# Performance work log

Measured on AMD Instinct MI355X. Metric: run time of the kernel, lower is better.

Reference implementation:

```python
import jax, jax.numpy as jnp
import numpy as np

LL = 1 << 20            # Fastfood padded size (power of 2 >= DD)
DD = 1024 * 768         # out_features * in_features
OUT, IN = 1024, 768


def fwht(v):
    """Unnormalized fast Walsh-Hadamard transform over a length-2^k vector."""
    n = v.shape[0]
    h = 1
    while h < n:
        v = v.reshape(-1, 2, h)
        v = jnp.concatenate([v[:, 0] + v[:, 1], v[:, 0] - v[:, 1]], axis=-1)
        h *= 2
    return v.reshape(n)


def setup_inputs() -> dict:
    key = jax.random.key(0)
    ks = jax.random.split(key, 7)
    x = jax.random.normal(ks[0], (8, 2048, IN), dtype=jnp.float32)
    theta = jax.random.normal(ks[1], (2048,), dtype=jnp.float32)
    W_0 = jax.random.normal(ks[2], (OUT, IN), dtype=jnp.float32) * 0.02
    b = jax.random.normal(ks[3], (OUT,), dtype=jnp.float32) * 0.02
    # Rademacher +/-1 diagonal
    BB = (jax.random.bernoulli(ks[4], 0.5, (LL,)).astype(jnp.float32) * 2.0 - 1.0)
    GG = jax.random.normal(ks[5], (LL,), dtype=jnp.float32)
    Pi = jax.random.permutation(ks[6], LL).astype(jnp.int64)
    return {"x": x, "theta": theta, "W_0": W_0, "b": b, "BB": BB, "GG": GG, "Pi": Pi}


def reference(x, theta, W_0, b, BB, GG, Pi):
    # pad intrinsic parameter to LL (theta.numel() < LL branch)
    theta_pad = jnp.zeros((LL,), dtype=theta.dtype).at[: theta.shape[0]].set(theta)
    # Fastfood: H B theta -> permute -> G diag -> H
    v = fwht(BB * theta_pad)
    v = v[Pi] * GG
    v = fwht(v)
    divisor = jnp.sqrt(LL * jnp.sum(GG * GG))
    update_vec = v[:DD] / (divisor * np.sqrt(float(DD) / LL))
    W_eff = W_0 + update_vec.reshape(OUT, IN)
    return jnp.einsum("bsi,oi->bso", x, W_eff) + b
```

## Files before the change

kernel.cpp:

```cpp
#include <hip/hip_runtime.h>
#include <hip/hip_bf16.h>


#define LL (1 << 20)
#define DD (1024 * 768)
#define OUTF 1024
#define INF 768
#define MROWS 16384

typedef __attribute__((ext_vector_type(8))) short s16x8;
typedef __attribute__((ext_vector_type(4))) float f32x4;
typedef __attribute__((ext_vector_type(16))) float f32x16;

__device__ __forceinline__ unsigned short f2bf(float f) {
    union { float f; unsigned u; } v; v.f = f;
    unsigned r = v.u + 0x7FFF + ((v.u >> 16) & 1);
    return (unsigned short)(r >> 16);
}

__global__ void k3_gather_fwht_lo(const int* __restrict__ Pi, const float* __restrict__ GG,
                                  const float* __restrict__ BB, const float* __restrict__ theta,
                                  const float* __restrict__ X, ushort* __restrict__ XB,
                                  float* __restrict__ T, float* __restrict__ partial) {
    __shared__ float s[1024];
    __shared__ float r01s[2048];
    __shared__ float ws4[4];
    const int tid = threadIdx.x;
    const int row = blockIdx.x;
    const int4   pv = ((const int4*)Pi)[row * 256 + tid];
    const float4 gv = ((const float4*)GG)[row * 256 + tid];
    for (int j = tid; j < 2048; j += 256) r01s[j] = BB[j] * theta[j];
    for (int h = 1; h < 1024; h <<= 1) {
        __syncthreads();
        for (int w = tid; w < 1024; w += 256) {
            int rr = w >> 9;
            int b  = w & 511;
            int bh = b & (h - 1);
            int i  = ((b - bh) << 1) + bh + rr * 1024;
            float a = r01s[i], c = r01s[i + h];
            r01s[i] = a + c; r01s[i + h] = a - c;
        }
    }
    float g2 = gv.x * gv.x + gv.y * gv.y + gv.z * gv.z + gv.w * gv.w;
    #pragma unroll
    for (int o = 32; o > 0; o >>= 1) g2 += __shfl_down(g2, o, 64);
    if ((tid & 63) == 0) ws4[tid >> 6] = g2;
    __syncthreads();
    {
        int p; float g, v;
        p = pv.x; g = gv.x;
        v = (r01s[p & 1023] + (((p >> 10) & 1) ? -1.0f : 1.0f) * r01s[1024 + (p & 1023)]) * g;
        s[tid * 4 + 0] = v;
        p = pv.y; g = gv.y;
        v = (r01s[p & 1023] + (((p >> 10) & 1) ? -1.0f : 1.0f) * r01s[1024 + (p & 1023)]) * g;
        s[tid * 4 + 1] = v;
        p = pv.z; g = gv.z;
        v = (r01s[p & 1023] + (((p >> 10) & 1) ? -1.0f : 1.0f) * r01s[1024 + (p & 1023)]) * g;
        s[tid * 4 + 2] = v;
        p = pv.w; g = gv.w;
        v = (r01s[p & 1023] + (((p >> 10) & 1) ? -1.0f : 1.0f) * r01s[1024 + (p & 1023)]) * g;
        s[tid * 4 + 3] = v;
    }
    for (int h = 1; h < 1024; h <<= 1) {
        __syncthreads();
        for (int w = tid; w < 512; w += 256) {
            int bh = w & (h - 1);
            int i  = ((w - bh) << 1) + bh;
            float a = s[i], c = s[i + h];
            s[i] = a + c; s[i + h] = a - c;
        }
    }
    __syncthreads();
    float4 v;
    v.x = s[tid * 4 + 0]; v.y = s[tid * 4 + 1]; v.z = s[tid * 4 + 2]; v.w = s[tid * 4 + 3];
    ((float4*)T)[row * 256 + tid] = v;
    if (tid == 0) partial[row] = ws4[0] + ws4[1] + ws4[2] + ws4[3];

    const float4* X4 = (const float4*)X + (size_t)row * 3072;
    ushort4* XB4 = (ushort4*)XB + (size_t)row * 3072;
    #pragma unroll
    for (int j = 0; j < 12; j++) {
        float4 xv = X4[j * 256 + tid];
        ushort4 o;
        o.x = f2bf(xv.x); o.y = f2bf(xv.y); o.z = f2bf(xv.z); o.w = f2bf(xv.w);
        XB4[j * 256 + tid] = o;
    }
}

__global__ void k4_fwht_hi(const float* __restrict__ T, const float* __restrict__ partial,
                           const float* __restrict__ W0, ushort* __restrict__ WB) {
    __shared__ float s[8 * 1025];
    __shared__ float rw[5];
    const int tid = threadIdx.x;
    float p = partial[tid] + partial[tid + 256] + partial[tid + 512] + partial[tid + 768];
    #pragma unroll
    for (int o = 32; o > 0; o >>= 1) p += __shfl_down(p, o, 64);
    if ((tid & 63) == 0) rw[tid >> 6] = p;

    const int lo0 = blockIdx.x * 8;
    const float4* T4 = (const float4*)T;
    const int hio = tid >> 1;
    const int q   = tid & 1;
    for (int hb = 0; hb < 8; hb++) {
        int hi = hb * 128 + hio;
        float4 v = T4[hi * 256 + (lo0 >> 2) + q];
        s[(4 * q + 0) * 1025 + hi] = v.x;
        s[(4 * q + 1) * 1025 + hi] = v.y;
        s[(4 * q + 2) * 1025 + hi] = v.z;
        s[(4 * q + 3) * 1025 + hi] = v.w;
    }
    __syncthreads();
    if (tid == 0) rw[4] = rw[0] + rw[1] + rw[2] + rw[3];
    for (int h = 1; h < 1024; h <<= 1) {
        for (int w = tid; w < 8 * 512; w += 256) {
            int col = w >> 9;
            int b   = w & 511;
            int bh  = b & (h - 1);
            int i   = ((b - bh) << 1) + bh;
            float* pp = s + col * 1025;
            float a = pp[i], c = pp[i + h];
            pp[i] = a + c; pp[i + h] = a - c;
        }
        __syncthreads();
    }
    const float scale = rsqrtf(rw[4] * (float)DD);
    for (int hb = 0; hb < 6; hb++) {
        int hi = hb * 128 + hio;
        int d  = hi * 1024 + lo0 + 4 * q;
        float4 w = *(const float4*)&W0[d];
        ushort4 o;
        o.x = f2bf(w.x + s[(4 * q + 0) * 1025 + hi] * scale);
        o.y = f2bf(w.y + s[(4 * q + 1) * 1025 + hi] * scale);
        o.z = f2bf(w.z + s[(4 * q + 2) * 1025 + hi] * scale);
        o.w = f2bf(w.w + s[(4 * q + 3) * 1025 + hi] * scale);
        *(ushort4*)&WB[d] = o;
    }
}

#define BM 128
#define BN 128
#define BK 64

__global__ __launch_bounds__(256)
void k7_gemm(const ushort* __restrict__ A, const ushort* __restrict__ B,
             const float* __restrict__ bias, float* __restrict__ C) {
    __shared__ ushort As[BM * BK];
    __shared__ ushort Bs[BN * BK];
    const int tid  = threadIdx.x;
    const int lane = tid & 63;
    const int wave = tid >> 6;
    const int m0 = blockIdx.x * BM;
    const int n0 = blockIdx.y * BN;
    const int wm = (wave & 1) * 64;
    const int wn = (wave >> 1) * 64;

    const int fr_row = lane & 31;
    const int fr_kh  = lane >> 5;

    f32x16 acc[2][2];
    #pragma unroll
    for (int i = 0; i < 2; i++)
        #pragma unroll
        for (int j = 0; j < 2; j++) acc[i][j] = (f32x16)(0.0f);

    for (int kt = 0; kt < INF; kt += BK) {
        #pragma unroll
        for (int i = 0; i < 4; i++) {
            const int s   = i * 256 + tid;
            const int row = s >> 3;
            const int kc  = (s & 7) ^ (row & 7);
            const ushort* ga = A + (size_t)(m0 + row) * INF + kt + kc * 8;
            const ushort* gb = B + (size_t)(n0 + row) * INF + kt + kc * 8;
            __builtin_amdgcn_global_load_lds(
                (const __attribute__((address_space(1))) void*)ga,
                (__attribute__((address_space(3))) void*)&As[i * 2048 + wave * 512], 16, 0, 0);
            __builtin_amdgcn_global_load_lds(
                (const __attribute__((address_space(1))) void*)gb,
                (__attribute__((address_space(3))) void*)&Bs[i * 2048 + wave * 512], 16, 0, 0);
        }
        __syncthreads();

        #pragma unroll
        for (int ks = 0; ks < 4; ks++) {
            const int kc = ks * 2 + fr_kh;
            s16x8 af[2], bf[2];
            #pragma unroll
            for (int mi = 0; mi < 2; mi++) {
                const int r = wm + mi * 32 + fr_row;
                af[mi] = *(const s16x8*)&As[(r * 8 + (kc ^ (r & 7))) * 8];
            }
            #pragma unroll
            for (int ni = 0; ni < 2; ni++) {
                const int r = wn + ni * 32 + fr_row;
                bf[ni] = *(const s16x8*)&Bs[(r * 8 + (kc ^ (r & 7))) * 8];
            }
            #pragma unroll
            for (int mi = 0; mi < 2; mi++)
                #pragma unroll
                for (int ni = 0; ni < 2; ni++)
                    acc[mi][ni] = __builtin_amdgcn_mfma_f32_32x32x16_bf16(
                        af[mi], bf[ni], acc[mi][ni], 0, 0, 0);
        }
        __syncthreads();
    }

    const int ccol = lane & 31;
    const int rbase = (lane >> 5) * 4;
    #pragma unroll
    for (int ni = 0; ni < 2; ni++) {
        const int n = n0 + wn + ni * 32 + ccol;
        const float bv = bias[n];
        #pragma unroll
        for (int mi = 0; mi < 2; mi++) {
            const int mb = m0 + wm + mi * 32 + rbase;
            #pragma unroll
            for (int r = 0; r < 16; r++) {
                const int m = mb + (r & 3) + 8 * (r >> 2);
                C[(size_t)m * OUTF + n] = acc[mi][ni][r] + bv;
            }
        }
    }
}

extern "C" void kernel_launch(void* const* d_in, const int* in_sizes, int n_in,
                              void* d_out, int out_size, void* d_ws, size_t ws_size,
                              hipStream_t stream) {
    (void)in_sizes; (void)n_in; (void)out_size; (void)ws_size;
    const float* x     = (const float*)d_in[0];
    const float* theta = (const float*)d_in[1];
    const float* W0    = (const float*)d_in[2];
    const float* bias  = (const float*)d_in[3];
    const float* BB    = (const float*)d_in[4];
    const float* GG    = (const float*)d_in[5];
    const int*   Pi    = (const int*)d_in[6];
    float* out = (float*)d_out;

    char* ws = (char*)d_ws;
    ushort* XB   = (ushort*)ws;
    float*  T    = (float*)(ws + 25165824);
    ushort* WB   = (ushort*)(ws + 29360128);
    float*  PART = (float*)(ws + 30932992);

    k3_gather_fwht_lo<<<1024, 256, 0, stream>>>(Pi, GG, BB, theta, x, XB, T, PART);
    k4_fwht_hi<<<128, 256, 0, stream>>>(T, PART, W0, WB);
    k7_gemm  <<<dim3(MROWS/BM, OUTF/BN), 256, 0, stream>>>(XB, WB, bias, out);
}
```

Before: 176.2 us.

## Fuse x fp32-to-bf16 conversion into GEMM A-tile loads; halve fwht_hi block width

The separate pass that converts x to bf16 inside the FWHT kernel is removed. The GEMM now reads fp32 x straight into registers, converts it with packed bf16 instructions and stores it to LDS, prefetching the next K tile in registers. This drops the 25MB bf16 round-trip through global memory. In exchange, x is re-read in fp32 by each of the 8 N-block columns, and the A loads are no longer async-to-LDS, which adds register pressure. The hi-FWHT kernel is also reshaped to 4 columns per block with 256 blocks, for more parallelism.

```diff
diff --git a/kernel.cpp b/kernel.cpp
--- a/kernel.cpp
+++ b/kernel.cpp
@@ -18,9 +18,14 @@
     return (unsigned short)(r >> 16);
 }
 
+__device__ __forceinline__ unsigned cvt_pk_bf16(float lo, float hi) {
+    unsigned r;
+    asm("v_cvt_pk_bf16_f32 %0, %1, %2" : "=v"(r) : "v"(lo), "v"(hi));
+    return r;
+}
+
 __global__ void k3_gather_fwht_lo(const int* __restrict__ Pi, const float* __restrict__ GG,
                                   const float* __restrict__ BB, const float* __restrict__ theta,
-                                  const float* __restrict__ X, ushort* __restrict__ XB,
                                   float* __restrict__ T, float* __restrict__ partial) {
     __shared__ float s[1024];
     __shared__ float r01s[2048];
@@ -75,21 +80,11 @@
     v.x = s[tid * 4 + 0]; v.y = s[tid * 4 + 1]; v.z = s[tid * 4 + 2]; v.w = s[tid * 4 + 3];
     ((float4*)T)[row * 256 + tid] = v;
     if (tid == 0) partial[row] = ws4[0] + ws4[1] + ws4[2] + ws4[3];
-
-    const float4* X4 = (const float4*)X + (size_t)row * 3072;
-    ushort4* XB4 = (ushort4*)XB + (size_t)row * 3072;
-    #pragma unroll
-    for (int j = 0; j < 12; j++) {
-        float4 xv = X4[j * 256 + tid];
-        ushort4 o;
-        o.x = f2bf(xv.x); o.y = f2bf(xv.y); o.z = f2bf(xv.z); o.w = f2bf(xv.w);
-        XB4[j * 256 + tid] = o;
-    }
 }
 
 __global__ void k4_fwht_hi(const float* __restrict__ T, const float* __restrict__ partial,
                            const float* __restrict__ W0, ushort* __restrict__ WB) {
-    __shared__ float s[8 * 1025];
+    __shared__ float s[4 * 1025];
     __shared__ float rw[5];
     const int tid = threadIdx.x;
     float p = partial[tid] + partial[tid + 256] + partial[tid + 512] + partial[tid + 768];
@@ -97,22 +92,21 @@
     for (int o = 32; o > 0; o >>= 1) p += __shfl_down(p, o, 64);
     if ((tid & 63) == 0) rw[tid >> 6] = p;
 
-    const int lo0 = blockIdx.x * 8;
+    const int lo0 = blockIdx.x * 4;
     const float4* T4 = (const float4*)T;
-    const int hio = tid >> 1;
-    const int q   = tid & 1;
-    for (int hb = 0; hb < 8; hb++) {
-        int hi = hb * 128 + hio;
-        float4 v = T4[hi * 256 + (lo0 >> 2) + q];
-        s[(4 * q + 0) * 1025 + hi] = v.x;
-        s[(4 * q + 1) * 1025 + hi] = v.y;
-        s[(4 * q + 2) * 1025 + hi] = v.z;
-        s[(4 * q + 3) * 1025 + hi] = v.w;
+    #pragma unroll
+    for (int hb = 0; hb < 4; hb++) {
+        int hi = hb * 256 + tid;
+        float4 v = T4[hi * 256 + (lo0 >> 2)];
+        s[0 * 1025 + hi] = v.x;
+        s[1 * 1025 + hi] = v.y;
+        s[2 * 1025 + hi] = v.z;
+        s[3 * 1025 + hi] = v.w;
     }
     __syncthreads();
     if (tid == 0) rw[4] = rw[0] + rw[1] + rw[2] + rw[3];
     for (int h = 1; h < 1024; h <<= 1) {
-        for (int w = tid; w < 8 * 512; w += 256) {
+        for (int w = tid; w < 4 * 512; w += 256) {
             int col = w >> 9;
             int b   = w & 511;
             int bh  = b & (h - 1);
@@ -124,15 +118,16 @@
         __syncthreads();
     }
     const float scale = rsqrtf(rw[4] * (float)DD);
-    for (int hb = 0; hb < 6; hb++) {
-        int hi = hb * 128 + hio;
-        int d  = hi * 1024 + lo0 + 4 * q;
+    #pragma unroll
+    for (int hb = 0; hb < 3; hb++) {
+        int hi = hb * 256 + tid;
+        int d  = hi * 1024 + lo0;
         float4 w = *(const float4*)&W0[d];
         ushort4 o;
-        o.x = f2bf(w.x + s[(4 * q + 0) * 1025 + hi] * scale);
-        o.y = f2bf(w.y + s[(4 * q + 1) * 1025 + hi] * scale);
-        o.z = f2bf(w.z + s[(4 * q + 2) * 1025 + hi] * scale);
-        o.w = f2bf(w.w + s[(4 * q + 3) * 1025 + hi] * scale);
+        o.x = f2bf(w.x + s[0 * 1025 + hi] * scale);
+        o.y = f2bf(w.y + s[1 * 1025 + hi] * scale);
+        o.z = f2bf(w.z + s[2 * 1025 + hi] * scale);
+        o.w = f2bf(w.w + s[3 * 1025 + hi] * scale);
         *(ushort4*)&WB[d] = o;
     }
 }
@@ -142,7 +137,7 @@
 #define BK 64
 
 __global__ __launch_bounds__(256)
-void k7_gemm(const ushort* __restrict__ A, const ushort* __restrict__ B,
+void k7_gemm(const float* __restrict__ A, const ushort* __restrict__ B,
              const float* __restrict__ bias, float* __restrict__ C) {
     __shared__ ushort As[BM * BK];
     __shared__ ushort Bs[BN * BK];
@@ -163,22 +158,54 @@
         #pragma unroll
         for (int j = 0; j < 2; j++) acc[i][j] = (f32x16)(0.0f);
 
+    int arow[4], akc[4];
+    #pragma unroll
+    for (int j = 0; j < 4; j++) {
+        const int s = j * 256 + tid;
+        arow[j] = s >> 3;
+        akc[j]  = (s & 7) ^ (arow[j] & 7);
+    }
+
+    f32x4 ar[8];
+    #pragma unroll
+    for (int j = 0; j < 4; j++) {
+        const float* ga = A + (size_t)(m0 + arow[j]) * INF + akc[j] * 8;
+        ar[2 * j]     = *(const f32x4*)ga;
+        ar[2 * j + 1] = *(const f32x4*)(ga + 4);
+    }
+
     for (int kt = 0; kt < INF; kt += BK) {
         #pragma unroll
         for (int i = 0; i < 4; i++) {
             const int s   = i * 256 + tid;
             const int row = s >> 3;
             const int kc  = (s & 7) ^ (row & 7);
-            const ushort* ga = A + (size_t)(m0 + row) * INF + kt + kc * 8;
             const ushort* gb = B + (size_t)(n0 + row) * INF + kt + kc * 8;
-            __builtin_amdgcn_global_load_lds(
-                (const __attribute__((address_space(1))) void*)ga,
-                (__attribute__((address_space(3))) void*)&As[i * 2048 + wave * 512], 16, 0, 0);
             __builtin_amdgcn_global_load_lds(
                 (const __attribute__((address_space(1))) void*)gb,
                 (__attribute__((address_space(3))) void*)&Bs[i * 2048 + wave * 512], 16, 0, 0);
         }
-        __syncthreads();
+        #pragma unroll
+        for (int j = 0; j < 4; j++) {
+            union { s16x8 v; unsigned u[4]; } o;
+            const f32x4 lo = ar[2 * j], hi = ar[2 * j + 1];
+            o.u[0] = cvt_pk_bf16(lo.x, lo.y);
+            o.u[1] = cvt_pk_bf16(lo.z, lo.w);
+            o.u[2] = cvt_pk_bf16(hi.x, hi.y);
+            o.u[3] = cvt_pk_bf16(hi.z, hi.w);
+            *(s16x8*)&As[(j * 256 + tid) * 8] = o.v;
+        }
+        __syncthreads();
+
+        if (kt + BK < INF) {
+            const int ktn = kt + BK;
+            #pragma unroll
+            for (int j = 0; j < 4; j++) {
+                const float* ga = A + (size_t)(m0 + arow[j]) * INF + ktn + akc[j] * 8;
+                ar[2 * j]     = *(const f32x4*)ga;
+                ar[2 * j + 1] = *(const f32x4*)(ga + 4);
+            }
+        }
 
         #pragma unroll
         for (int ks = 0; ks < 4; ks++) {
@@ -236,12 +263,11 @@
     float* out = (float*)d_out;
 
     char* ws = (char*)d_ws;
-    ushort* XB   = (ushort*)ws;
-    float*  T    = (float*)(ws + 25165824);
-    ushort* WB   = (ushort*)(ws + 29360128);
-    float*  PART = (float*)(ws + 30932992);
-
-    k3_gather_fwht_lo<<<1024, 256, 0, stream>>>(Pi, GG, BB, theta, x, XB, T, PART);
-    k4_fwht_hi<<<128, 256, 0, stream>>>(T, PART, W0, WB);
-    k7_gemm  <<<dim3(MROWS/BM, OUTF/BN), 256, 0, stream>>>(XB, WB, bias, out);
-}
+    float*  T    = (float*)ws;
+    ushort* WB   = (ushort*)(ws + 4194304);
+    float*  PART = (float*)(ws + 5767168);
+
+    k3_gather_fwht_lo<<<1024, 256, 0, stream>>>(Pi, GG, BB, theta, T, PART);
+    k4_fwht_hi<<<256, 256, 0, stream>>>(T, PART, W0, WB);
+    k7_gemm  <<<dim3(MROWS/BM, OUTF/BN), 256, 0, stream>>>(x, WB, bias, out);
+}
```

After: 179.4 us. About the same (+1.8%).

## Restructure Fastfood transforms with register/shuffle FWHT and split cast kernel

Applied to the files above, without the earlier changes.

The 2048-point r01 transform is hoisted into its own single-block kernel so it is no longer recomputed in every row block. The x-to-bf16 cast moves into a separate streaming kernel that uses packed bf16 conversion. Both FWHT stages now run first in registers, then through wave shuffles, then a single radix-4 shared-memory pass, replacing ten barrier-separated shared-memory butterfly passes. The intermediate is written in a transposed layout so the high-stage kernel reads contiguous float4 columns, at the cost of extra kernel launches.

```diff
diff --git a/kernel.cpp b/kernel.cpp
--- a/kernel.cpp
+++ b/kernel.cpp
@@ -18,121 +18,226 @@
     return (unsigned short)(r >> 16);
 }
 
-__global__ void k3_gather_fwht_lo(const int* __restrict__ Pi, const float* __restrict__ GG,
-                                  const float* __restrict__ BB, const float* __restrict__ theta,
-                                  const float* __restrict__ X, ushort* __restrict__ XB,
-                                  float* __restrict__ T, float* __restrict__ partial) {
-    __shared__ float s[1024];
+__device__ __forceinline__ unsigned cvt_pk_bf16(float lo, float hi) {
+    unsigned r;
+    asm("v_cvt_pk_bf16_f32 %0, %1, %2" : "=v"(r) : "v"(lo), "v"(hi));
+    return r;
+}
+
+__global__ void k0_r01(const float* __restrict__ BB, const float* __restrict__ theta,
+                       float* __restrict__ r01g) {
+    __shared__ float sx[2048];
+    const int t = threadIdx.x;
+    const int r = t >> 7, tt = t & 127, lane = t & 63;
+    float v[8];
+    {
+        const float4 a0 = *(const float4*)&BB[r * 1024 + tt * 8];
+        const float4 a1 = *(const float4*)&BB[r * 1024 + tt * 8 + 4];
+        const float4 b0 = *(const float4*)&theta[r * 1024 + tt * 8];
+        const float4 b1 = *(const float4*)&theta[r * 1024 + tt * 8 + 4];
+        v[0] = a0.x * b0.x; v[1] = a0.y * b0.y; v[2] = a0.z * b0.z; v[3] = a0.w * b0.w;
+        v[4] = a1.x * b1.x; v[5] = a1.y * b1.y; v[6] = a1.z * b1.z; v[7] = a1.w * b1.w;
+    }
+    float a;
+    a = v[0]; v[0] = a + v[1]; v[1] = a - v[1];
+    a = v[2]; v[2] = a + v[3]; v[3] = a - v[3];
+    a = v[4]; v[4] = a + v[5]; v[5] = a - v[5];
+    a = v[6]; v[6] = a + v[7]; v[7] = a - v[7];
+    a = v[0]; v[0] = a + v[2]; v[2] = a - v[2];
+    a = v[1]; v[1] = a + v[3]; v[3] = a - v[3];
+    a = v[4]; v[4] = a + v[6]; v[6] = a - v[6];
+    a = v[5]; v[5] = a + v[7]; v[7] = a - v[7];
+    a = v[0]; v[0] = a + v[4]; v[4] = a - v[4];
+    a = v[1]; v[1] = a + v[5]; v[5] = a - v[5];
+    a = v[2]; v[2] = a + v[6]; v[6] = a - v[6];
+    a = v[3]; v[3] = a + v[7]; v[7] = a - v[7];
+    #pragma unroll
+    for (int j = 0; j < 6; j++) {
+        const float sgn = ((lane >> j) & 1) ? -1.0f : 1.0f;
+        #pragma unroll
+        for (int c = 0; c < 8; c++) {
+            float o = __shfl_xor(v[c], 1 << j, 64);
+            v[c] = fmaf(sgn, v[c], o);
+        }
+    }
+    #pragma unroll
+    for (int c = 0; c < 8; c++) sx[r * 1024 + tt * 8 + c] = v[c];
+    __syncthreads();
+    {
+        const int pt = r * 1024 + (tt ^ 64) * 8;
+        const float sgn = (tt & 64) ? -1.0f : 1.0f;
+        #pragma unroll
+        for (int c = 0; c < 8; c++) v[c] = fmaf(sgn, v[c], sx[pt + c]);
+    }
+    #pragma unroll
+    for (int c = 0; c < 8; c++) r01g[r * 1024 + tt * 8 + c] = v[c];
+}
+
+__global__ void k1_cast(const float* __restrict__ X, ushort* __restrict__ XB) {
+    const f32x4* X4 = (const f32x4*)X;
+    s16x8* O = (s16x8*)XB;
+    size_t i = (size_t)blockIdx.x * 256 + threadIdx.x;
+    #pragma unroll
+    for (int j = 0; j < 3; j++, i += 524288) {
+        const f32x4 A = X4[2 * i];
+        const f32x4 B = X4[2 * i + 1];
+        union { s16x8 v; unsigned u[4]; } o;
+        o.u[0] = cvt_pk_bf16(A.x, A.y);
+        o.u[1] = cvt_pk_bf16(A.z, A.w);
+        o.u[2] = cvt_pk_bf16(B.x, B.y);
+        o.u[3] = cvt_pk_bf16(B.z, B.w);
+        O[i] = o.v;
+    }
+}
+
+__global__ __launch_bounds__(1024)
+void k3_gather_fwht_lo(const int* __restrict__ Pi, const float* __restrict__ GG,
+                       const float* __restrict__ r01g, f32x4* __restrict__ T2,
+                       float* __restrict__ partial) {
     __shared__ float r01s[2048];
-    __shared__ float ws4[4];
-    const int tid = threadIdx.x;
-    const int row = blockIdx.x;
-    const int4   pv = ((const int4*)Pi)[row * 256 + tid];
-    const float4 gv = ((const float4*)GG)[row * 256 + tid];
-    for (int j = tid; j < 2048; j += 256) r01s[j] = BB[j] * theta[j];
-    for (int h = 1; h < 1024; h <<= 1) {
-        __syncthreads();
-        for (int w = tid; w < 1024; w += 256) {
-            int rr = w >> 9;
-            int b  = w & 511;
-            int bh = b & (h - 1);
-            int i  = ((b - bh) << 1) + bh + rr * 1024;
-            float a = r01s[i], c = r01s[i + h];
-            r01s[i] = a + c; r01s[i + h] = a - c;
-        }
-    }
+    __shared__ f32x4 sA[1024];
+    __shared__ float sB[4 * 1028];
+    __shared__ float ws[16];
+    const int t = threadIdx.x;
+    const int s_r = t >> 8, tt = t & 255, lane = t & 63;
+    const int row = blockIdx.x * 4 + s_r;
+
+    r01s[t] = r01g[t];
+    r01s[t + 1024] = r01g[t + 1024];
+    const int4   pv = ((const int4*)Pi)[row * 256 + tt];
+    const float4 gv = ((const float4*)GG)[row * 256 + tt];
     float g2 = gv.x * gv.x + gv.y * gv.y + gv.z * gv.z + gv.w * gv.w;
     #pragma unroll
     for (int o = 32; o > 0; o >>= 1) g2 += __shfl_down(g2, o, 64);
-    if ((tid & 63) == 0) ws4[tid >> 6] = g2;
-    __syncthreads();
-    {
-        int p; float g, v;
+    if (lane == 0) ws[t >> 6] = g2;
+    __syncthreads();
+
+    float v[4];
+    {
+        int p; float g;
         p = pv.x; g = gv.x;
-        v = (r01s[p & 1023] + (((p >> 10) & 1) ? -1.0f : 1.0f) * r01s[1024 + (p & 1023)]) * g;
-        s[tid * 4 + 0] = v;
+        v[0] = (r01s[p & 1023] + (((p >> 10) & 1) ? -1.0f : 1.0f) * r01s[1024 + (p & 1023)]) * g;
         p = pv.y; g = gv.y;
-        v = (r01s[p & 1023] + (((p >> 10) & 1) ? -1.0f : 1.0f) * r01s[1024 + (p & 1023)]) * g;
-        s[tid * 4 + 1] = v;
+        v[1] = (r01s[p & 1023] + (((p >> 10) & 1) ? -1.0f : 1.0f) * r01s[1024 + (p & 1023)]) * g;
         p = pv.z; g = gv.z;
-        v = (r01s[p & 1023] + (((p >> 10) & 1) ? -1.0f : 1.0f) * r01s[1024 + (p & 1023)]) * g;
-        s[tid * 4 + 2] = v;
+        v[2] = (r01s[p & 1023] + (((p >> 10) & 1) ? -1.0f : 1.0f) * r01s[1024 + (p & 1023)]) * g;
         p = pv.w; g = gv.w;
-        v = (r01s[p & 1023] + (((p >> 10) & 1) ? -1.0f : 1.0f) * r01s[1024 + (p & 1023)]) * g;
-        s[tid * 4 + 3] = v;
-    }
-    for (int h = 1; h < 1024; h <<= 1) {
-        __syncthreads();
-        for (int w = tid; w < 512; w += 256) {
-            int bh = w & (h - 1);
-            int i  = ((w - bh) << 1) + bh;
-            float a = s[i], c = s[i + h];
-            s[i] = a + c; s[i + h] = a - c;
-        }
-    }
-    __syncthreads();
-    float4 v;
-    v.x = s[tid * 4 + 0]; v.y = s[tid * 4 + 1]; v.z = s[tid * 4 + 2]; v.w = s[tid * 4 + 3];
-    ((float4*)T)[row * 256 + tid] = v;
-    if (tid == 0) partial[row] = ws4[0] + ws4[1] + ws4[2] + ws4[3];
-
-    const float4* X4 = (const float4*)X + (size_t)row * 3072;
-    ushort4* XB4 = (ushort4*)XB + (size_t)row * 3072;
-    #pragma unroll
-    for (int j = 0; j < 12; j++) {
-        float4 xv = X4[j * 256 + tid];
+        v[3] = (r01s[p & 1023] + (((p >> 10) & 1) ? -1.0f : 1.0f) * r01s[1024 + (p & 1023)]) * g;
+    }
+    float a;
+    a = v[0]; v[0] = a + v[1]; v[1] = a - v[1];
+    a = v[2]; v[2] = a + v[3]; v[3] = a - v[3];
+    a = v[0]; v[0] = a + v[2]; v[2] = a - v[2];
+    a = v[1]; v[1] = a + v[3]; v[3] = a - v[3];
+    #pragma unroll
+    for (int j = 0; j < 6; j++) {
+        const float sgn = ((lane >> j) & 1) ? -1.0f : 1.0f;
+        #pragma unroll
+        for (int c = 0; c < 4; c++) {
+            float o = __shfl_xor(v[c], 1 << j, 64);
+            v[c] = fmaf(sgn, v[c], o);
+        }
+    }
+    {
+        f32x4 vv; vv.x = v[0]; vv.y = v[1]; vv.z = v[2]; vv.w = v[3];
+        sA[t] = vv;
+    }
+    __syncthreads();
+    {
+        const int b = t & ~192;
+        const f32x4 q00 = sA[b];
+        const f32x4 q10 = sA[b + 64];
+        const f32x4 q01 = sA[b + 128];
+        const f32x4 q11 = sA[b + 192];
+        const float s8 = (tt & 64) ? -1.0f : 1.0f;
+        const float s9 = (tt & 128) ? -1.0f : 1.0f;
+        #pragma unroll
+        for (int c = 0; c < 4; c++)
+            v[c] = (q00[c] + s9 * q01[c]) + s8 * (q10[c] + s9 * q11[c]);
+    }
+    if (t == 0) {
+        float s = 0;
+        #pragma unroll
+        for (int i = 0; i < 16; i++) s += ws[i];
+        partial[blockIdx.x] = s;
+    }
+    {
+        f32x4 vv; vv.x = v[0]; vv.y = v[1]; vv.z = v[2]; vv.w = v[3];
+        *(f32x4*)&sB[s_r * 1028 + 4 * tt] = vv;
+    }
+    __syncthreads();
+    {
+        const int rl = t & 3;
+        const int lo4 = t >> 2;
+        const f32x4 w = *(const f32x4*)&sB[rl * 1028 + lo4 * 4];
+        T2[(size_t)lo4 * 1024 + blockIdx.x * 4 + rl] = w;
+    }
+}
+
+__global__ __launch_bounds__(1024)
+void k4_fwht_hi(const f32x4* __restrict__ T2, const float* __restrict__ partial,
+                const float* __restrict__ W0, ushort* __restrict__ WB) {
+    __shared__ f32x4 sx[1024];
+    __shared__ float rw[17];
+    const int t = threadIdx.x;
+    const int g = blockIdx.x;
+    const int lane = t & 63;
+
+    float pr = 0.0f;
+    if (t < 256) pr = partial[t];
+    #pragma unroll
+    for (int o = 32; o > 0; o >>= 1) pr += __shfl_down(pr, o, 64);
+    if (t < 256 && lane == 0) rw[t >> 6] = pr;
+
+    f32x4 vv = T2[(size_t)g * 1024 + t];
+    #pragma unroll
+    for (int j = 0; j < 6; j++) {
+        const float sgn = ((lane >> j) & 1) ? -1.0f : 1.0f;
+        #pragma unroll
+        for (int c = 0; c < 4; c++) {
+            float o = __shfl_xor(vv[c], 1 << j, 64);
+            vv[c] = fmaf(sgn, vv[c], o);
+        }
+    }
+    sx[t] = vv;
+    __syncthreads();
+    if (t == 0) rw[16] = rw[0] + rw[1] + rw[2] + rw[3];
+    {
+        const int b = t & ~192;
+        const f32x4 q00 = sx[b];
+        const f32x4 q10 = sx[b + 64];
+        const f32x4 q01 = sx[b + 128];
+        const f32x4 q11 = sx[b + 192];
+        const float s6 = (t & 64) ? -1.0f : 1.0f;
+        const float s7 = (t & 128) ? -1.0f : 1.0f;
+        #pragma unroll
+        for (int c = 0; c < 4; c++)
+            vv[c] = (q00[c] + s7 * q01[c]) + s6 * (q10[c] + s7 * q11[c]);
+    }
+    __syncthreads();
+    sx[t] = vv;
+    __syncthreads();
+    {
+        const int b = t & ~768;
+        const f32x4 q00 = sx[b];
+        const f32x4 q10 = sx[b + 256];
+        const f32x4 q01 = sx[b + 512];
+        const f32x4 q11 = sx[b + 768];
+        const float s8 = (t & 256) ? -1.0f : 1.0f;
+        const float s9 = (t & 512) ? -1.0f : 1.0f;
+        #pragma unroll
+        for (int c = 0; c < 4; c++)
+            vv[c] = (q00[c] + s9 * q01[c]) + s8 * (q10[c] + s9 * q11[c]);
+    }
+    if (t < 768) {
+        const float scale = rsqrtf(rw[16] * (float)DD);
+        const size_t d = (size_t)t * 1024 + 4 * g;
+        const float4 w = *(const float4*)&W0[d];
         ushort4 o;
-        o.x = f2bf(xv.x); o.y = f2bf(xv.y); o.z = f2bf(xv.z); o.w = f2bf(xv.w);
-        XB4[j * 256 + tid] = o;
-    }
-}
-
-__global__ void k4_fwht_hi(const float* __restrict__ T, const float* __restrict__ partial,
-                           const float* __restrict__ W0, ushort* __restrict__ WB) {
-    __shared__ float s[8 * 1025];
-    __shared__ float rw[5];
-    const int tid = threadIdx.x;
-    float p = partial[tid] + partial[tid + 256] + partial[tid + 512] + partial[tid + 768];
-    #pragma unroll
-    for (int o = 32; o > 0; o >>= 1) p += __shfl_down(p, o, 64);
-    if ((tid & 63) == 0) rw[tid >> 6] = p;
-
-    const int lo0 = blockIdx.x * 8;
-    const float4* T4 = (const float4*)T;
-    const int hio = tid >> 1;
-    const int q   = tid & 1;
-    for (int hb = 0; hb < 8; hb++) {
-        int hi = hb * 128 + hio;
-        float4 v = T4[hi * 256 + (lo0 >> 2) + q];
-        s[(4 * q + 0) * 1025 + hi] = v.x;
-        s[(4 * q + 1) * 1025 + hi] = v.y;
-        s[(4 * q + 2) * 1025 + hi] = v.z;
-        s[(4 * q + 3) * 1025 + hi] = v.w;
-    }
-    __syncthreads();
-    if (tid == 0) rw[4] = rw[0] + rw[1] + rw[2] + rw[3];
-    for (int h = 1; h < 1024; h <<= 1) {
-        for (int w = tid; w < 8 * 512; w += 256) {
-            int col = w >> 9;
-            int b   = w & 511;
-            int bh  = b & (h - 1);
-            int i   = ((b - bh) << 1) + bh;
-            float* pp = s + col * 1025;
-            float a = pp[i], c = pp[i + h];
-            pp[i] = a + c; pp[i + h] = a - c;
-        }
-        __syncthreads();
-    }
-    const float scale = rsqrtf(rw[4] * (float)DD);
-    for (int hb = 0; hb < 6; hb++) {
-        int hi = hb * 128 + hio;
-        int d  = hi * 1024 + lo0 + 4 * q;
-        float4 w = *(const float4*)&W0[d];
-        ushort4 o;
-        o.x = f2bf(w.x + s[(4 * q + 0) * 1025 + hi] * scale);
-        o.y = f2bf(w.y + s[(4 * q + 1) * 1025 + hi] * scale);
-        o.z = f2bf(w.z + s[(4 * q + 2) * 1025 + hi] * scale);
-        o.w = f2bf(w.w + s[(4 * q + 3) * 1025 + hi] * scale);
+        o.x = f2bf(w.x + vv.x * scale);
+        o.y = f2bf(w.y + vv.y * scale);
+        o.z = f2bf(w.z + vv.z * scale);
+        o.w = f2bf(w.w + vv.w * scale);
         *(ushort4*)&WB[d] = o;
     }
 }
@@ -237,11 +342,14 @@
 
     char* ws = (char*)d_ws;
     ushort* XB   = (ushort*)ws;
-    float*  T    = (float*)(ws + 25165824);
+    f32x4*  T2   = (f32x4*)(ws + 25165824);
     ushort* WB   = (ushort*)(ws + 29360128);
-    float*  PART = (float*)(ws + 30932992);
-
-    k3_gather_fwht_lo<<<1024, 256, 0, stream>>>(Pi, GG, BB, theta, x, XB, T, PART);
-    k4_fwht_hi<<<128, 256, 0, stream>>>(T, PART, W0, WB);
-    k7_gemm  <<<dim3(MROWS/BM, OUTF/BN), 256, 0, stream>>>(XB, WB, bias, out);
-}
+    float*  R01  = (float*)(ws + 30932992);
+    float*  PART = (float*)(ws + 30941184);
+
+    k0_r01          <<<1,    256, 0, stream>>>(BB, theta, R01);
+    k1_cast         <<<2048, 256, 0, stream>>>(x, XB);
+    k3_gather_fwht_lo<<<256, 1024, 0, stream>>>(Pi, GG, R01, T2, PART);
+    k4_fwht_hi      <<<256, 1024, 0, stream>>>(T2, PART, W0, WB);
+    k7_gemm<<<dim3(MROWS/BM, OUTF/BN), 256, 0, stream>>>(XB, WB, bias, out);
+}
```

Measured after the change: 170.9 us. -3.0%, faster.
